# Kernel optimization log

Hardware: AMD Instinct MI355X
Metric: run time of the kernel (lower is better)

Reference implementation:

```python
import jax, jax.numpy as jnp
import numpy as np
from jax import lax

NC1, NC2, NC3 = 64, 64, 512
TEMP = 1.0
EPS = 1e-5
B = 256


def setup_inputs() -> dict:
    key = jax.random.key(0)
    ks = jax.random.split(key, 16)
    d = {}
    d["inp"] = jax.random.normal(ks[0], (B, 3, 32, 32), jnp.float32)
    d["conv1_w"] = jax.random.normal(ks[1], (6, 3, 5, 5), jnp.float32) * 0.1
    d["conv1_b"] = jax.random.normal(ks[2], (6,), jnp.float32) * 0.1
    d["bn1_g"] = jnp.ones((6,), jnp.float32)
    d["bn1_b"] = jnp.zeros((6,), jnp.float32)
    d["conv2_w"] = jax.random.normal(ks[3], (16, 6, 5, 5), jnp.float32) * 0.1
    d["conv2_b"] = jax.random.normal(ks[4], (16,), jnp.float32) * 0.1
    d["bn2_g"] = jnp.ones((16,), jnp.float32)
    d["bn2_b"] = jnp.zeros((16,), jnp.float32)
    d["fc1_w"] = jax.random.normal(ks[5], (120, 400), jnp.float32) * 0.05
    d["fc1_b"] = jax.random.normal(ks[6], (120,), jnp.float32) * 0.05
    d["fc2_w"] = jax.random.normal(ks[7], (10, 120), jnp.float32) * 0.05
    d["fc2_b"] = jax.random.normal(ks[8], (10,), jnp.float32) * 0.05
    d["k1s"] = jax.random.normal(ks[9], (NC1, 6), jnp.float32)
    d["k2s"] = jax.random.normal(ks[10], (NC2, 16), jnp.float32)
    d["k3s"] = jax.random.normal(ks[11], (NC3, 120), jnp.float32)
    return d


def _conv(x, w, b):
    y = lax.conv_general_dilated(x, w, (1, 1), 'VALID',
                                 dimension_numbers=('NCHW', 'OIHW', 'NCHW'))
    return y + b[None, :, None, None]


def _bn_train(x, g, b):
    # BatchNorm2d in training mode: biased batch stats over (N,H,W)
    mean = x.mean(axis=(0, 2, 3), keepdims=True)
    var = ((x - mean) ** 2).mean(axis=(0, 2, 3), keepdims=True)
    return (x - mean) / jnp.sqrt(var + EPS) * g[None, :, None, None] + b[None, :, None, None]


def _maxpool2(x):
    return lax.reduce_window(x, -jnp.inf, lax.max, (1, 1, 2, 2), (1, 1, 2, 2), 'VALID')


def _codebook_logits_spatial(act, keys):
    # act: [B,C,H,W], keys: [K,C] -> -||act - k||_2 over C -> [B,K,H,W]
    diff = act[:, None] - keys[None, :, :, None, None]
    return -jnp.sqrt((diff ** 2).sum(axis=2))


def _neural_gas_loss(v, temp):
    n_clusters = v.shape[1]
    weightings = jnp.exp(-jnp.arange(n_clusters, dtype=v.dtype) / temp)
    sorted_v = jnp.sort(v, axis=1)
    return (sorted_v ** 2 * weightings).sum(axis=1)


def reference(inp, conv1_w, conv1_b, bn1_g, bn1_b, conv2_w, conv2_b, bn2_g, bn2_b,
              fc1_w, fc1_b, fc2_w, fc2_b, k1s, k2s, k3s):
    act1 = _bn_train(_conv(inp, conv1_w, conv1_b), bn1_g, bn1_b)          # [B,6,28,28]
    act_logits1 = _codebook_logits_spatial(act1, k1s)                     # [B,NC1,28,28]
    x = _maxpool2(jax.nn.relu(act1))                                      # [B,6,14,14]
    act2 = _bn_train(_conv(x, conv2_w, conv2_b), bn2_g, bn2_b)            # [B,16,10,10]
    act_logits2 = _codebook_logits_spatial(act2, k2s)                     # [B,NC2,10,10]
    x = _maxpool2(jax.nn.relu(act2))                                      # [B,16,5,5]
    x = x.reshape(x.shape[0], -1)                                         # [B,400]
    act3 = x @ fc1_w.T + fc1_b                                            # [B,120]
    diff3 = act3[:, None, :] - k3s[None, :, :]
    act_logits3 = -jnp.sqrt((diff3 ** 2).sum(axis=2))                     # [B,NC3]
    x = jax.nn.relu(act3)
    act4 = x @ fc2_w.T + fc2_b                                            # [B,10]
    # ARGS.ng branch: neural-gas cluster loss + argmax assignments
    cluster_loss = _neural_gas_loss(act_logits3, TEMP)                    # [B]
    assignments = jnp.argmax(act_logits3, axis=1)                         # [B] int
    return (assignments, cluster_loss.mean(), act4, act_logits1, act_logits2, act_logits3)
```

## Files before the change

kernel.cpp:

```cpp
#include <hip/hip_runtime.h>

#define B 256
#define EPSV 1e-5f

#define OFF_ASSIGN 0
#define OFF_LOSS   256
#define OFF_ACT4   257
#define OFF_L1     2817
#define OFF_L2     12847873
#define OFF_L3     14486273

__device__ __forceinline__ void wave_reduce2(float& s, float& q) {
#pragma unroll
    for (int o = 32; o > 0; o >>= 1) {
        s += __shfl_down(s, o, 64);
        q += __shfl_down(q, o, 64);
    }
}

__global__ __launch_bounds__(256) void conv1_kernel(
        const float* __restrict__ inp, const float* __restrict__ w,
        const float* __restrict__ bias, float* __restrict__ c1,
        float* __restrict__ part,
        const float* __restrict__ w1, const float* __restrict__ k3,
        float* __restrict__ w1t, float* __restrict__ k3st) {
    int bc = blockIdx.x;
    int tid = threadIdx.x;
    if (bc >= 1536) {
        int idx = (bc - 1536) * 256 + tid;
        if (idx < 48000) {
            int c = idx / 120, o = idx % 120;
            w1t[idx] = w1[o * 400 + c];
        } else if (idx < 48000 + 61440) {
            int j = idx - 48000;
            int c = j >> 9, k = j & 511;
            k3st[j] = k3[k * 120 + c];
        }
        return;
    }
    int b = bc / 6, c = bc % 6;
    __shared__ float ws[75];
    __shared__ float rs[4], rq[4];
    if (tid < 75) ws[tid] = w[c * 75 + tid];
    __syncthreads();
    const float* ip = inp + b * 3072;
    float bs = bias[c];
    float s = 0.f, sq = 0.f;
    for (int hw = tid; hw < 784; hw += 256) {
        int oh = hw / 28, ow = hw % 28;
        float acc = bs;
#pragma unroll
        for (int ic = 0; ic < 3; ++ic) {
            const float* ipc = ip + ic * 1024 + oh * 32 + ow;
            const float* wc = ws + ic * 25;
#pragma unroll
            for (int kh = 0; kh < 5; ++kh)
#pragma unroll
                for (int kw = 0; kw < 5; ++kw)
                    acc += ipc[kh * 32 + kw] * wc[kh * 5 + kw];
        }
        c1[bc * 784 + hw] = acc;
        s += acc; sq += acc * acc;
    }
    wave_reduce2(s, sq);
    if ((tid & 63) == 0) { rs[tid >> 6] = s; rq[tid >> 6] = sq; }
    __syncthreads();
    if (tid == 0) {
        part[bc * 2]     = rs[0] + rs[1] + rs[2] + rs[3];
        part[bc * 2 + 1] = rq[0] + rq[1] + rq[2] + rq[3];
    }
}

__global__ __launch_bounds__(1024) void stage1_kernel(
        const float* __restrict__ c1raw, const float* __restrict__ part1,
        const float* __restrict__ g1, const float* __restrict__ bb1,
        const float* __restrict__ k1s,
        const float* __restrict__ c2w, const float* __restrict__ c2b,
        float* __restrict__ out, float* __restrict__ c2raw,
        float* __restrict__ part2) {
    int b = blockIdx.x, tid = threadIdx.x;
    int lane = tid & 63, wid = tid >> 6;
    __shared__ __align__(16) float act[4704];
    __shared__ float sk1[384], k2sq1[64];
    __shared__ float w2s[2400];
    __shared__ float xp[1176];
    __shared__ __align__(16) float sa[1600];
    __shared__ float chs[6], chq[6], ssc[6], ssh[6];
    if (wid < 6) {
        float s = 0.f, q = 0.f;
#pragma unroll
        for (int j = 0; j < 4; ++j) {
            int bi = lane + 64 * j;
            s += part1[(bi * 6 + wid) * 2];
            q += part1[(bi * 6 + wid) * 2 + 1];
        }
        wave_reduce2(s, q);
        if (lane == 0) { chs[wid] = s; chq[wid] = q; }
    }
    if (tid >= 640 && tid < 1024) sk1[tid - 640] = k1s[tid - 640];
    for (int i = tid; i < 2400; i += 1024) w2s[i] = c2w[i];
    __syncthreads();
    if (tid < 6) {
        float m = chs[tid] * (1.f / 200704.f);
        float v = chq[tid] * (1.f / 200704.f) - m * m;
        float sc = g1[tid] * rsqrtf(v + EPSV);
        ssc[tid] = sc; ssh[tid] = bb1[tid] - m * sc;
    }
    if (tid >= 64 && tid < 128) {
        int k = tid - 64;
        float s = 0.f;
#pragma unroll
        for (int c = 0; c < 6; ++c) { float x = sk1[k * 6 + c]; s += x * x; }
        k2sq1[k] = s;
    }
    __syncthreads();
    for (int i = tid; i < 4704; i += 1024) {
        int c = i / 784;
        act[i] = c1raw[b * 4704 + i] * ssc[c] + ssh[c];
    }
    __syncthreads();
    if (tid < 784) {
        float a0 = act[tid], a1 = act[784 + tid], a2 = act[1568 + tid];
        float a3 = act[2352 + tid], a4 = act[3136 + tid], a5 = act[3920 + tid];
        float A2 = a0*a0 + a1*a1 + a2*a2 + a3*a3 + a4*a4 + a5*a5;
        float* op = out + OFF_L1 + (long)b * 50176 + tid;
#pragma unroll 4
        for (int k = 0; k < 64; ++k) {
            const float* kp = sk1 + k * 6;
            float dot = a0*kp[0] + a1*kp[1] + a2*kp[2] + a3*kp[3] + a4*kp[4] + a5*kp[5];
            *op = -sqrtf(fmaxf(A2 + k2sq1[k] - 2.f * dot, 0.f));
            op += 784;
        }
    } else {
        for (int i = tid - 784; i < 1176; i += 240) {
            int c = i / 196, p = i % 196, ph = p / 14, pw = p % 14;
            const float* ap = act + c * 784 + ph * 56 + pw * 2;
            float m = fmaxf(fmaxf(ap[0], ap[1]), fmaxf(ap[28], ap[29]));
            xp[i] = fmaxf(m, 0.f);
        }
    }
    __syncthreads();
    for (int i = tid; i < 1600; i += 1024) {
        int c = i / 100, hw = i - c * 100;
        int oh = hw / 10, ow = hw - oh * 10;
        float acc = c2b[c];
#pragma unroll
        for (int ic = 0; ic < 6; ++ic) {
            const float* xsrc = xp + ic * 196 + oh * 14 + ow;
            const float* wp = w2s + c * 150 + ic * 25;
#pragma unroll
            for (int kh = 0; kh < 5; ++kh)
#pragma unroll
                for (int kw = 0; kw < 5; ++kw)
                    acc += xsrc[kh * 14 + kw] * wp[kh * 5 + kw];
        }
        sa[i] = acc;
        c2raw[b * 1600 + i] = acc;
    }
    __syncthreads();
    {
        float s = 0.f, q = 0.f;
        if (lane < 100) { float x = sa[wid * 100 + lane]; s = x; q = x * x; }
        if (lane < 36)  { float x = sa[wid * 100 + 64 + lane]; s += x; q += x * x; }
        wave_reduce2(s, q);
        if (lane == 0) { part2[(b * 16 + wid) * 2] = s; part2[(b * 16 + wid) * 2 + 1] = q; }
    }
}

__global__ __launch_bounds__(1024) void stage2_kernel(
        const float* __restrict__ c2raw, const float* __restrict__ part2,
        const float* __restrict__ g2, const float* __restrict__ bb2,
        const float* __restrict__ k2s,
        const float* __restrict__ w1t, const float* __restrict__ f1b,
        const float* __restrict__ f2w, const float* __restrict__ f2b,
        const float* __restrict__ k3st,
        float* __restrict__ out, float* __restrict__ lossb) {
    int b = blockIdx.x, tid = threadIdx.x;
    int lane = tid & 63, wid = tid >> 6;
    __shared__ __align__(16) float sa[1600];
    __shared__ float sk2[1024], k2sq2[64];
    __shared__ float chs[16], chq[16], ssc[16], ssh[16];
    __shared__ float xs[400];
    __shared__ float partq[1024];
    __shared__ float a3r[120], a3p[120];
    __shared__ __align__(16) float sv[512];
    __shared__ __align__(16) float pv[1024];
    __shared__ int cntp[1024];
    __shared__ float wsum[8], wmv[8];
    __shared__ int wmi[8];
    {
        float s = 0.f, q = 0.f;
#pragma unroll
        for (int j = 0; j < 4; ++j) {
            int bi = lane + 64 * j;
            s += part2[(bi * 16 + wid) * 2];
            q += part2[(bi * 16 + wid) * 2 + 1];
        }
        wave_reduce2(s, q);
        if (lane == 0) { chs[wid] = s; chq[wid] = q; }
    }
    sk2[tid] = k2s[tid];
    __syncthreads();
    if (tid < 16) {
        float m = chs[tid] * (1.f / 25600.f);
        float v = chq[tid] * (1.f / 25600.f) - m * m;
        float sc = g2[tid] * rsqrtf(v + EPSV);
        ssc[tid] = sc; ssh[tid] = bb2[tid] - m * sc;
    }
    if (tid >= 64 && tid < 128) {
        int k = tid - 64;
        float s = 0.f;
#pragma unroll
        for (int c = 0; c < 16; ++c) { float x = sk2[k * 16 + c]; s += x * x; }
        k2sq2[k] = s;
    }
    __syncthreads();
    for (int i = tid; i < 1600; i += 1024) {
        int c = i / 100;
        sa[i] = c2raw[b * 1600 + i] * ssc[c] + ssh[c];
    }
    __syncthreads();
    if (tid < 800) {
        int kg = tid / 100, hw = tid - kg * 100;
        float a[16], A2 = 0.f;
#pragma unroll
        for (int c = 0; c < 16; ++c) { a[c] = sa[c * 100 + hw]; A2 += a[c] * a[c]; }
        float* op2 = out + OFF_L2 + (long)b * 6400 + kg * 800 + hw;
#pragma unroll
        for (int k = kg * 8; k < kg * 8 + 8; ++k) {
            const float* kp = sk2 + k * 16;
            float dot = 0.f;
#pragma unroll
            for (int c = 0; c < 16; ++c) dot += a[c] * kp[c];
            *op2 = -sqrtf(fmaxf(A2 + k2sq2[k] - 2.f * dot, 0.f));
            op2 += 100;
        }
    } else {
        for (int i = tid - 800; i < 400; i += 224) {
            int c = i / 25, p = i % 25, ph = p / 5, pw = p % 5;
            const float* ap = sa + c * 100 + ph * 20 + pw * 2;
            float m = fmaxf(fmaxf(ap[0], ap[1]), fmaxf(ap[10], ap[11]));
            xs[i] = fmaxf(m, 0.f);
        }
    }
    __syncthreads();
    {
        int o = tid & 127, q8 = tid >> 7;
        float s = 0.f;
        if (o < 120) {
            const float* wp = w1t + (q8 * 50) * 120 + o;
            const float* xq = xs + q8 * 50;
#pragma unroll 10
            for (int c = 0; c < 50; ++c) s += xq[c] * wp[c * 120];
        }
        partq[q8 * 128 + o] = s;
    }
    __syncthreads();
    if (tid < 120) {
        float acc = f1b[tid];
#pragma unroll
        for (int q8 = 0; q8 < 8; ++q8) acc += partq[q8 * 128 + tid];
        a3r[tid] = acc;
        a3p[tid] = fmaxf(acc, 0.f);
    }
    __syncthreads();
    {
        int k = tid & 511, h = tid >> 9;
        const float* kp = k3st + k;
        float s = 0.f;
#pragma unroll 6
        for (int c = h * 60; c < h * 60 + 60; ++c) {
            float d = a3r[c] - kp[c * 512];
            s += d * d;
        }
        pv[h * 512 + k] = s;
    }
    if (tid < 10) {
        float acc = f2b[tid];
        const float* wp = f2w + tid * 120;
#pragma unroll 8
        for (int c = 0; c < 120; ++c) acc += a3p[c] * wp[c];
        out[OFF_ACT4 + b * 10 + tid] = acc;
    }
    __syncthreads();
    if (tid < 512) {
        float v = -sqrtf(pv[tid] + pv[512 + tid]);
        sv[tid] = v;
        out[OFF_L3 + (long)b * 512 + tid] = v;
    }
    __syncthreads();
    {
        int i = tid & 511, h = tid >> 9;
        float v = sv[i];
        const float4* sv4 = reinterpret_cast<const float4*>(sv);
        int cnt = 0;
#pragma unroll 8
        for (int j4 = h * 64; j4 < h * 64 + 64; ++j4) {
            float4 o4 = sv4[j4];
            int jb = j4 * 4;
            cnt += (o4.x < v || (o4.x == v && jb < i)) ? 1 : 0;
            cnt += (o4.y < v || (o4.y == v && jb + 1 < i)) ? 1 : 0;
            cnt += (o4.z < v || (o4.z == v && jb + 2 < i)) ? 1 : 0;
            cnt += (o4.w < v || (o4.w == v && jb + 3 < i)) ? 1 : 0;
        }
        cntp[h * 512 + i] = cnt;
    }
    __syncthreads();
    if (tid < 512) {
        float v = sv[tid];
        int cnt = cntp[tid] + cntp[512 + tid];
        float contrib = v * v * expf(-(float)cnt);
        float ssum = contrib;
#pragma unroll
        for (int o = 32; o > 0; o >>= 1) ssum += __shfl_down(ssum, o, 64);
        float mv = v; int mi = tid;
#pragma unroll
        for (int o = 32; o > 0; o >>= 1) {
            float ov = __shfl_down(mv, o, 64);
            int oi = __shfl_down(mi, o, 64);
            if (ov > mv || (ov == mv && oi < mi)) { mv = ov; mi = oi; }
        }
        if (lane == 0) { wsum[wid] = ssum; wmv[wid] = mv; wmi[wid] = mi; }
    }
    __syncthreads();
    if (tid == 0) {
        float tot = 0.f;
        float bmv = wmv[0]; int bmi = wmi[0];
#pragma unroll
        for (int w = 0; w < 8; ++w) {
            tot += wsum[w];
            if (wmv[w] > bmv || (wmv[w] == bmv && wmi[w] < bmi)) { bmv = wmv[w]; bmi = wmi[w]; }
        }
        lossb[b] = tot;
        out[OFF_ASSIGN + b] = (float)bmi;
    }
}

__global__ void final_kernel(const float* __restrict__ loss_b, float* __restrict__ out_loss) {
    __shared__ float r[256];
    int tid = threadIdx.x;
    r[tid] = loss_b[tid];
    __syncthreads();
    for (int s = 128; s > 0; s >>= 1) {
        if (tid < s) r[tid] += r[tid + s];
        __syncthreads();
    }
    if (tid == 0) out_loss[0] = r[0] / 256.f;
}

extern "C" void kernel_launch(void* const* d_in, const int* in_sizes, int n_in,
                              void* d_out, int out_size, void* d_ws, size_t ws_size,
                              hipStream_t stream) {
    const float* inp = (const float*)d_in[0];
    const float* c1w = (const float*)d_in[1];
    const float* c1b = (const float*)d_in[2];
    const float* g1  = (const float*)d_in[3];
    const float* bb1 = (const float*)d_in[4];
    const float* c2w = (const float*)d_in[5];
    const float* c2b = (const float*)d_in[6];
    const float* g2  = (const float*)d_in[7];
    const float* bb2 = (const float*)d_in[8];
    const float* f1w = (const float*)d_in[9];
    const float* f1b = (const float*)d_in[10];
    const float* f2w = (const float*)d_in[11];
    const float* f2b = (const float*)d_in[12];
    const float* k1  = (const float*)d_in[13];
    const float* k2  = (const float*)d_in[14];
    const float* k3  = (const float*)d_in[15];
    float* out = (float*)d_out;

    float* W = (float*)d_ws;
    float* c1raw = W;
    float* part1 = c1raw + 1204224;
    float* c2raw = part1 + 3072;
    float* part2 = c2raw + 409600;
    float* lossb = part2 + 8192;
    float* w1t   = lossb + 256;
    float* k3st  = w1t + 48000;

    conv1_kernel<<<1964, 256, 0, stream>>>(inp, c1w, c1b, c1raw, part1,
                                           f1w, k3, w1t, k3st);
    stage1_kernel<<<B, 1024, 0, stream>>>(c1raw, part1, g1, bb1, k1, c2w, c2b,
                                          out, c2raw, part2);
    stage2_kernel<<<B, 1024, 0, stream>>>(c2raw, part2, g2, bb2, k2,
                                          w1t, f1b, f2w, f2b, k3st, out, lossb);
    final_kernel<<<1, 256, 0, stream>>>(lossb, out + OFF_LOSS);
}
```

Baseline: 91.79 us.

## Precompute augmented codebooks, overlap conv2 with logits, fuse final loss reduction

Codebook squared norms for k1s and k2s are now computed once in an extra conv1 block instead of per-block in shared memory. conv1 reads weights directly from global memory, dropping its shared copy and barrier. In stage1, the pooling runs first, then the codebook-logit waves and conv2 waves (wave-per-4-channels with shuffle reductions) run concurrently. Stage2 redistributes the codebook-logit work across all waves, and the final mean-loss kernel is folded into stage2 via an atomic last-block counter. This removes one launch and some redundant shared-memory staging, but needs a memset on every call and adds atomic ordering complexity.

```diff
diff --git a/kernel.cpp b/kernel.cpp
--- a/kernel.cpp
+++ b/kernel.cpp
@@ -23,9 +23,36 @@
         const float* __restrict__ bias, float* __restrict__ c1,
         float* __restrict__ part,
         const float* __restrict__ w1, const float* __restrict__ k3,
-        float* __restrict__ w1t, float* __restrict__ k3st) {
+        const float* __restrict__ k1s, const float* __restrict__ k2s,
+        float* __restrict__ w1t, float* __restrict__ k3st,
+        float* __restrict__ k1aug, float* __restrict__ k2aug) {
     int bc = blockIdx.x;
     int tid = threadIdx.x;
+    if (bc == 1964) {
+        if (tid < 64) {
+            float K2 = 0.f;
+#pragma unroll
+            for (int c = 0; c < 6; ++c) {
+                float x = k1s[tid * 6 + c];
+                k1aug[tid * 8 + c] = x;
+                K2 += x * x;
+            }
+            k1aug[tid * 8 + 6] = K2;
+            k1aug[tid * 8 + 7] = 0.f;
+        } else if (tid < 128) {
+            int k = tid - 64;
+            float K2 = 0.f;
+#pragma unroll
+            for (int c = 0; c < 16; ++c) {
+                float x = k2s[k * 16 + c];
+                k2aug[k * 20 + c] = x;
+                K2 += x * x;
+            }
+            k2aug[k * 20 + 16] = K2;
+            k2aug[k * 20 + 17] = 0.f; k2aug[k * 20 + 18] = 0.f; k2aug[k * 20 + 19] = 0.f;
+        }
+        return;
+    }
     if (bc >= 1536) {
         int idx = (bc - 1536) * 256 + tid;
         if (idx < 48000) {
@@ -39,11 +66,9 @@
         return;
     }
     int b = bc / 6, c = bc % 6;
-    __shared__ float ws[75];
     __shared__ float rs[4], rq[4];
-    if (tid < 75) ws[tid] = w[c * 75 + tid];
-    __syncthreads();
     const float* ip = inp + b * 3072;
+    const float* wc = w + c * 75;
     float bs = bias[c];
     float s = 0.f, sq = 0.f;
     for (int hw = tid; hw < 784; hw += 256) {
@@ -52,12 +77,12 @@
 #pragma unroll
         for (int ic = 0; ic < 3; ++ic) {
             const float* ipc = ip + ic * 1024 + oh * 32 + ow;
-            const float* wc = ws + ic * 25;
+            const float* wp = wc + ic * 25;
 #pragma unroll
             for (int kh = 0; kh < 5; ++kh)
 #pragma unroll
                 for (int kw = 0; kw < 5; ++kw)
-                    acc += ipc[kh * 32 + kw] * wc[kh * 5 + kw];
+                    acc += ipc[kh * 32 + kw] * wp[kh * 5 + kw];
         }
         c1[bc * 784 + hw] = acc;
         s += acc; sq += acc * acc;
@@ -74,17 +99,14 @@
 __global__ __launch_bounds__(1024) void stage1_kernel(
         const float* __restrict__ c1raw, const float* __restrict__ part1,
         const float* __restrict__ g1, const float* __restrict__ bb1,
-        const float* __restrict__ k1s,
+        const float* __restrict__ k1aug,
         const float* __restrict__ c2w, const float* __restrict__ c2b,
         float* __restrict__ out, float* __restrict__ c2raw,
         float* __restrict__ part2) {
     int b = blockIdx.x, tid = threadIdx.x;
     int lane = tid & 63, wid = tid >> 6;
     __shared__ __align__(16) float act[4704];
-    __shared__ float sk1[384], k2sq1[64];
-    __shared__ float w2s[2400];
     __shared__ float xp[1176];
-    __shared__ __align__(16) float sa[1600];
     __shared__ float chs[6], chq[6], ssc[6], ssh[6];
     if (wid < 6) {
         float s = 0.f, q = 0.f;
@@ -97,8 +119,6 @@
         wave_reduce2(s, q);
         if (lane == 0) { chs[wid] = s; chq[wid] = q; }
     }
-    if (tid >= 640 && tid < 1024) sk1[tid - 640] = k1s[tid - 640];
-    for (int i = tid; i < 2400; i += 1024) w2s[i] = c2w[i];
     __syncthreads();
     if (tid < 6) {
         float m = chs[tid] * (1.f / 200704.f);
@@ -106,79 +126,96 @@
         float sc = g1[tid] * rsqrtf(v + EPSV);
         ssc[tid] = sc; ssh[tid] = bb1[tid] - m * sc;
     }
-    if (tid >= 64 && tid < 128) {
-        int k = tid - 64;
-        float s = 0.f;
-#pragma unroll
-        for (int c = 0; c < 6; ++c) { float x = sk1[k * 6 + c]; s += x * x; }
-        k2sq1[k] = s;
-    }
     __syncthreads();
     for (int i = tid; i < 4704; i += 1024) {
         int c = i / 784;
         act[i] = c1raw[b * 4704 + i] * ssc[c] + ssh[c];
     }
     __syncthreads();
-    if (tid < 784) {
-        float a0 = act[tid], a1 = act[784 + tid], a2 = act[1568 + tid];
-        float a3 = act[2352 + tid], a4 = act[3136 + tid], a5 = act[3920 + tid];
+    for (int i = tid; i < 1176; i += 1024) {
+        int c = i / 196, p = i % 196, ph = p / 14, pw = p % 14;
+        const float* ap = act + c * 784 + ph * 56 + pw * 2;
+        float m = fmaxf(fmaxf(ap[0], ap[1]), fmaxf(ap[28], ap[29]));
+        xp[i] = fmaxf(m, 0.f);
+    }
+    __syncthreads();
+    if (tid < 768) {
+        int hw = tid;
+        float a0 = act[hw], a1 = act[784 + hw], a2 = act[1568 + hw];
+        float a3 = act[2352 + hw], a4 = act[3136 + hw], a5 = act[3920 + hw];
         float A2 = a0*a0 + a1*a1 + a2*a2 + a3*a3 + a4*a4 + a5*a5;
-        float* op = out + OFF_L1 + (long)b * 50176 + tid;
+        bool two = (tid < 16);
+        int hw2 = 768 + tid;
+        float b0 = 0.f, b1 = 0.f, b2 = 0.f, b3 = 0.f, b4 = 0.f, b5 = 0.f, B2 = 0.f;
+        if (two) {
+            b0 = act[hw2]; b1 = act[784 + hw2]; b2 = act[1568 + hw2];
+            b3 = act[2352 + hw2]; b4 = act[3136 + hw2]; b5 = act[3920 + hw2];
+            B2 = b0*b0 + b1*b1 + b2*b2 + b3*b3 + b4*b4 + b5*b5;
+        }
+        float* op = out + OFF_L1 + (long)b * 50176;
 #pragma unroll 4
         for (int k = 0; k < 64; ++k) {
-            const float* kp = sk1 + k * 6;
-            float dot = a0*kp[0] + a1*kp[1] + a2*kp[2] + a3*kp[3] + a4*kp[4] + a5*kp[5];
-            *op = -sqrtf(fmaxf(A2 + k2sq1[k] - 2.f * dot, 0.f));
-            op += 784;
+            const float* kp = k1aug + k * 8;
+            float k0 = kp[0], k1 = kp[1], k2 = kp[2];
+            float k3 = kp[3], k4 = kp[4], k5 = kp[5], K2 = kp[6];
+            float dot = a0*k0 + a1*k1 + a2*k2 + a3*k3 + a4*k4 + a5*k5;
+            op[k * 784 + hw] = -sqrtf(fmaxf(A2 + K2 - 2.f * dot, 0.f));
+            if (two) {
+                float dot2 = b0*k0 + b1*k1 + b2*k2 + b3*k3 + b4*k4 + b5*k5;
+                op[k * 784 + hw2] = -sqrtf(fmaxf(B2 + K2 - 2.f * dot2, 0.f));
+            }
         }
     } else {
-        for (int i = tid - 784; i < 1176; i += 240) {
-            int c = i / 196, p = i % 196, ph = p / 14, pw = p % 14;
-            const float* ap = act + c * 784 + ph * 56 + pw * 2;
-            float m = fmaxf(fmaxf(ap[0], ap[1]), fmaxf(ap[28], ap[29]));
-            xp[i] = fmaxf(m, 0.f);
-        }
-    }
-    __syncthreads();
-    for (int i = tid; i < 1600; i += 1024) {
-        int c = i / 100, hw = i - c * 100;
-        int oh = hw / 10, ow = hw - oh * 10;
-        float acc = c2b[c];
-#pragma unroll
-        for (int ic = 0; ic < 6; ++ic) {
-            const float* xsrc = xp + ic * 196 + oh * 14 + ow;
-            const float* wp = w2s + c * 150 + ic * 25;
-#pragma unroll
-            for (int kh = 0; kh < 5; ++kh)
-#pragma unroll
-                for (int kw = 0; kw < 5; ++kw)
-                    acc += xsrc[kh * 14 + kw] * wp[kh * 5 + kw];
-        }
-        sa[i] = acc;
-        c2raw[b * 1600 + i] = acc;
-    }
-    __syncthreads();
-    {
-        float s = 0.f, q = 0.f;
-        if (lane < 100) { float x = sa[wid * 100 + lane]; s = x; q = x * x; }
-        if (lane < 36)  { float x = sa[wid * 100 + 64 + lane]; s += x; q += x * x; }
-        wave_reduce2(s, q);
-        if (lane == 0) { part2[(b * 16 + wid) * 2] = s; part2[(b * 16 + wid) * 2 + 1] = q; }
+        int w4 = __builtin_amdgcn_readfirstlane(wid - 12);
+        int base0 = (lane / 10) * 14 + (lane % 10);
+        int hw2 = 64 + lane;
+        int base1 = (hw2 / 10) * 14 + (hw2 % 10);
+        bool l36 = (lane < 36);
+#pragma unroll
+        for (int j = 0; j < 4; ++j) {
+            int c = w4 * 4 + j;
+            const float* wp = c2w + c * 150;
+            float bias2 = c2b[c];
+            float v0 = bias2, v1 = bias2;
+#pragma unroll
+            for (int ic = 0; ic < 6; ++ic) {
+                const float* xb = xp + ic * 196;
+                const float* wpc = wp + ic * 25;
+#pragma unroll
+                for (int kh = 0; kh < 5; ++kh)
+#pragma unroll
+                    for (int kw = 0; kw < 5; ++kw) {
+                        float wgt = wpc[kh * 5 + kw];
+                        v0 += xb[base0 + kh * 14 + kw] * wgt;
+                        if (l36) v1 += xb[base1 + kh * 14 + kw] * wgt;
+                    }
+            }
+            c2raw[b * 1600 + c * 100 + lane] = v0;
+            if (l36) c2raw[b * 1600 + c * 100 + hw2] = v1;
+            float s = v0 + (l36 ? v1 : 0.f) * 0.f;
+            s = v0 + (l36 ? v1 : 0.f);
+            float q = v0 * v0 + (l36 ? v1 * v1 : 0.f);
+            wave_reduce2(s, q);
+            if (lane == 0) {
+                part2[(b * 16 + c) * 2]     = s;
+                part2[(b * 16 + c) * 2 + 1] = q;
+            }
+        }
     }
 }
 
 __global__ __launch_bounds__(1024) void stage2_kernel(
         const float* __restrict__ c2raw, const float* __restrict__ part2,
         const float* __restrict__ g2, const float* __restrict__ bb2,
-        const float* __restrict__ k2s,
+        const float* __restrict__ k2aug,
         const float* __restrict__ w1t, const float* __restrict__ f1b,
         const float* __restrict__ f2w, const float* __restrict__ f2b,
         const float* __restrict__ k3st,
-        float* __restrict__ out, float* __restrict__ lossb) {
+        float* __restrict__ out, float* __restrict__ lossb,
+        unsigned* __restrict__ done) {
     int b = blockIdx.x, tid = threadIdx.x;
     int lane = tid & 63, wid = tid >> 6;
     __shared__ __align__(16) float sa[1600];
-    __shared__ float sk2[1024], k2sq2[64];
     __shared__ float chs[16], chq[16], ssc[16], ssh[16];
     __shared__ float xs[400];
     __shared__ float partq[1024];
@@ -188,6 +225,7 @@
     __shared__ int cntp[1024];
     __shared__ float wsum[8], wmv[8];
     __shared__ int wmi[8];
+    __shared__ int lastflag;
     {
         float s = 0.f, q = 0.f;
 #pragma unroll
@@ -199,7 +237,6 @@
         wave_reduce2(s, q);
         if (lane == 0) { chs[wid] = s; chq[wid] = q; }
     }
-    sk2[tid] = k2s[tid];
     __syncthreads();
     if (tid < 16) {
         float m = chs[tid] * (1.f / 25600.f);
@@ -207,36 +244,33 @@
         float sc = g2[tid] * rsqrtf(v + EPSV);
         ssc[tid] = sc; ssh[tid] = bb2[tid] - m * sc;
     }
-    if (tid >= 64 && tid < 128) {
-        int k = tid - 64;
-        float s = 0.f;
-#pragma unroll
-        for (int c = 0; c < 16; ++c) { float x = sk2[k * 16 + c]; s += x * x; }
-        k2sq2[k] = s;
-    }
     __syncthreads();
     for (int i = tid; i < 1600; i += 1024) {
         int c = i / 100;
         sa[i] = c2raw[b * 1600 + i] * ssc[c] + ssh[c];
     }
     __syncthreads();
-    if (tid < 800) {
-        int kg = tid / 100, hw = tid - kg * 100;
-        float a[16], A2 = 0.f;
-#pragma unroll
-        for (int c = 0; c < 16; ++c) { a[c] = sa[c * 100 + hw]; A2 += a[c] * a[c]; }
-        float* op2 = out + OFF_L2 + (long)b * 6400 + kg * 800 + hw;
-#pragma unroll
-        for (int k = kg * 8; k < kg * 8 + 8; ++k) {
-            const float* kp = sk2 + k * 16;
-            float dot = 0.f;
-#pragma unroll
-            for (int c = 0; c < 16; ++c) dot += a[c] * kp[c];
-            *op2 = -sqrtf(fmaxf(A2 + k2sq2[k] - 2.f * dot, 0.f));
-            op2 += 100;
-        }
-    } else {
-        for (int i = tid - 800; i < 400; i += 224) {
+    {
+        int kb = __builtin_amdgcn_readfirstlane(wid) * 4;
+#pragma unroll
+        for (int r = 0; r < 2; ++r) {
+            int hw = r * 64 + lane;
+            if (hw < 100) {
+                float a[16]; float A2 = 0.f;
+#pragma unroll
+                for (int c = 0; c < 16; ++c) { a[c] = sa[c * 100 + hw]; A2 += a[c] * a[c]; }
+                float* ob = out + OFF_L2 + (long)b * 6400 + hw;
+#pragma unroll
+                for (int kk = 0; kk < 4; ++kk) {
+                    const float* kp = k2aug + (kb + kk) * 20;
+                    float dot = 0.f;
+#pragma unroll
+                    for (int c = 0; c < 16; ++c) dot += a[c] * kp[c];
+                    ob[(kb + kk) * 100] = -sqrtf(fmaxf(A2 + kp[16] - 2.f * dot, 0.f));
+                }
+            }
+        }
+        for (int i = tid; i < 400; i += 1024) {
             int c = i / 25, p = i % 25, ph = p / 5, pw = p % 5;
             const float* ap = sa + c * 100 + ph * 20 + pw * 2;
             float m = fmaxf(fmaxf(ap[0], ap[1]), fmaxf(ap[10], ap[11]));
@@ -333,19 +367,21 @@
         }
         lossb[b] = tot;
         out[OFF_ASSIGN + b] = (float)bmi;
-    }
-}
-
-__global__ void final_kernel(const float* __restrict__ loss_b, float* __restrict__ out_loss) {
-    __shared__ float r[256];
-    int tid = threadIdx.x;
-    r[tid] = loss_b[tid];
-    __syncthreads();
-    for (int s = 128; s > 0; s >>= 1) {
-        if (tid < s) r[tid] += r[tid + s];
+        __threadfence();
+        unsigned r = __hip_atomic_fetch_add(done, 1u, __ATOMIC_ACQ_REL, __HIP_MEMORY_SCOPE_AGENT);
+        lastflag = (r == (unsigned)(gridDim.x - 1)) ? 1 : 0;
+    }
+    __syncthreads();
+    if (lastflag) {
+        float* rf = pv;
+        if (tid < 256) rf[tid] = lossb[tid];
         __syncthreads();
-    }
-    if (tid == 0) out_loss[0] = r[0] / 256.f;
+        for (int s2 = 128; s2 > 0; s2 >>= 1) {
+            if (tid < s2) rf[tid] += rf[tid + s2];
+            __syncthreads();
+        }
+        if (tid == 0) out[OFF_LOSS] = rf[0] * (1.f / 256.f);
+    }
 }
 
 extern "C" void kernel_launch(void* const* d_in, const int* in_sizes, int n_in,
@@ -370,19 +406,22 @@
     float* out = (float*)d_out;
 
     float* W = (float*)d_ws;
-    float* c1raw = W;
-    float* part1 = c1raw + 1204224;
-    float* c2raw = part1 + 3072;
-    float* part2 = c2raw + 409600;
-    float* lossb = part2 + 8192;
-    float* w1t   = lossb + 256;
-    float* k3st  = w1t + 48000;
-
-    conv1_kernel<<<1964, 256, 0, stream>>>(inp, c1w, c1b, c1raw, part1,
-                                           f1w, k3, w1t, k3st);
-    stage1_kernel<<<B, 1024, 0, stream>>>(c1raw, part1, g1, bb1, k1, c2w, c2b,
+    unsigned* done = (unsigned*)d_ws;
+    float* part1 = W + 64;
+    float* c1raw = W + 3136;
+    float* c2raw = W + 1207360;
+    float* part2 = W + 1616960;
+    float* lossb = W + 1625152;
+    float* w1t   = W + 1625408;
+    float* k3st  = W + 1673408;
+    float* k1aug = W + 1734848;
+    float* k2aug = W + 1735360;
+
+    hipMemsetAsync(d_ws, 0, 64, stream);
+    conv1_kernel<<<1965, 256, 0, stream>>>(inp, c1w, c1b, c1raw, part1,
+                                           f1w, k3, k1, k2, w1t, k3st, k1aug, k2aug);
+    stage1_kernel<<<B, 1024, 0, stream>>>(c1raw, part1, g1, bb1, k1aug, c2w, c2b,
                                           out, c2raw, part2);
-    stage2_kernel<<<B, 1024, 0, stream>>>(c2raw, part2, g2, bb2, k2,
-                                          w1t, f1b, f2w, f2b, k3st, out, lossb);
-    final_kernel<<<1, 256, 0, stream>>>(lossb, out + OFF_LOSS);
+    stage2_kernel<<<B, 1024, 0, stream>>>(c2raw, part2, g2, bb2, k2aug,
+                                          w1t, f1b, f2w, f2b, k3st, out, lossb, done);
 }
```

After: 135.7 us. +47.8%, slower.
